# Kernel tuning notes

Hardware: AMD Instinct MI355X
Metric: run time of the kernel (lower is better)

The kernel has to match this reference:

```python
import jax, jax.numpy as jnp
import numpy as np

TAU = 1.0
K = 10
N_NODES = 1048576
N_GRAPHS = 4096


def setup_inputs() -> dict:
    key = jax.random.key(0)
    k1, k2, k3 = jax.random.split(key, 3)
    # per-node scalar logits
    x = jax.random.normal(k1, (N_NODES, 1), dtype=jnp.float32)
    # uniforms for gumbel noise, kept away from {0,1} for log stability
    uniforms = jax.random.uniform(k2, (N_NODES, 3 * K), dtype=jnp.float32,
                                  minval=1e-6, maxval=1.0 - 1e-6)
    # PyG-style ptr: B+1 cumulative offsets, ptr[0]=0, ptr[-1]=N
    cuts = jnp.sort(jax.random.randint(k3, (N_GRAPHS - 1,), 1, N_NODES))
    ptr = jnp.concatenate([jnp.zeros((1,), cuts.dtype), cuts,
                           jnp.full((1,), N_NODES, cuts.dtype)])
    return {"x": x, "uniforms": uniforms, "ptr": ptr}


def reference(x, uniforms, ptr):
    # x: [N, 1] node logits; uniforms: [N, 3k]; ptr: [B+1] segment offsets
    N = x.shape[0]
    B = ptr.shape[0] - 1
    # node i belongs to graph g where ptr[g] <= i < ptr[g+1]
    seg = jnp.searchsorted(ptr, jnp.arange(N), side="right") - 1  # [N]
    gumbel = -jnp.log(-jnp.log(uniforms))                           # [N, 3k]
    noisy = (gumbel + x) / TAU                                      # [N, 3k]
    # segmented softmax over nodes (dim=0 within each graph), per column
    m = jax.ops.segment_max(noisy, seg, num_segments=B)             # [B, 3k]
    e = jnp.exp(noisy - m[seg])                                     # [N, 3k]
    denom = jax.ops.segment_sum(e, seg, num_segments=B)             # [B, 3k]
    probs = e / denom[seg]                                          # [N, 3k]
    # max over the 3k gumbel samples per node
    samples = jnp.max(probs, axis=1)                                # [N]
    return samples[:, None]                                         # [N, 1]
```

## Files before the change

kernel.cpp:

```cpp
#include <hip/hip_runtime.h>

#define NK3 30
#define NKP 15

__device__ __forceinline__ float hw_log2(float a) { return __builtin_amdgcn_logf(a); }
__device__ __forceinline__ float hw_exp2(float a) { return __builtin_amdgcn_exp2f(a); }
__device__ __forceinline__ float hw_rcp(float a)  { return __builtin_amdgcn_rcpf(a); }

template <int CTRL>
__device__ __forceinline__ float dpp_add(float v) {
    int s = __builtin_amdgcn_update_dpp(0, __float_as_int(v), CTRL, 0xF, 0xF, true);
    return v + __int_as_float(s);
}
__device__ __forceinline__ float group16_sum(float v) {
    v = dpp_add<0xB1>(v);
    v = dpp_add<0x4E>(v);
    v = dpp_add<0x141>(v);
    v = dpp_add<0x140>(v);
    return v;
}


__global__ __launch_bounds__(256) void k1_window_sums(
    const float* __restrict__ x, const float* __restrict__ uniforms,
    float* __restrict__ wp16, int N)
{
    const int wid  = (blockIdx.x << 2) + (threadIdx.x >> 6);
    const int lane = threadIdx.x & 63;
    const int base0 = wid << 8;
    if (base0 >= N) return;

    for (int c = 0; c < 4; ++c) {
        const int base = base0 + (c << 6);
        if (base >= N) return;
        const int n  = base + lane;
        const int nv = (n < N) ? n : (N - 1);

        const float2* row = reinterpret_cast<const float2*>(uniforms + (size_t)nv * NK3);
        float2 u[NKP];
#pragma unroll
        for (int k = 0; k < NKP; ++k) u[k] = row[k];
        float E = hw_exp2(x[nv] * 1.44269504f);
        E = (n < N) ? E : 0.0f;

        float r[NK3];
#pragma unroll
        for (int k = 0; k < NKP; ++k) {
            r[2 * k]     = E * hw_rcp(-hw_log2(u[k].x));
            r[2 * k + 1] = E * hw_rcp(-hw_log2(u[k].y));
        }

#pragma unroll
        for (int j = 0; j < NK3; ++j) r[j] = group16_sum(r[j]);

        if ((lane & 15) == 0) {
            float* dst = wp16 + ((size_t)(base >> 4) + (lane >> 4)) * NK3;
#pragma unroll
            for (int j = 0; j < NK3; ++j) dst[j] = r[j];
        }
    }
}

__global__ __launch_bounds__(256) void k2_segment_den(
    const float* __restrict__ x, const float* __restrict__ uniforms,
    const int* __restrict__ ptr, const float* __restrict__ wp16,
    float* __restrict__ den, int B)
{
    const int s = (blockIdx.x << 2) + (threadIdx.x >> 6);
    if (s >= B) return;
    const int lane = threadIdx.x & 63;
    const int h  = lane >> 5;
    const int j  = lane & 31;
    const bool jact = (j < NK3);
    const int jc = jact ? j : 0;

    const int start = ptr[s];
    const int end   = ptr[s + 1];

    const int wlo = (start + 15) >> 4;
    const int whi = end >> 4;
    const int head_end = min(wlo << 4, end);
    const int tail_beg = max(whi << 4, head_end);

    float acc = 0.0f;

    for (int w = wlo + h; w < whi; w += 2)
        acc += wp16[(size_t)w * NK3 + jc];

    for (int n = start + h; n < head_end; n += 2) {
        const float E = hw_exp2(x[n] * 1.44269504f);
        const float uv = uniforms[(size_t)n * NK3 + jc];
        acc = fmaf(E, hw_rcp(-hw_log2(uv)), acc);
    }
    for (int n = tail_beg + h; n < end; n += 2) {
        const float E = hw_exp2(x[n] * 1.44269504f);
        const float uv = uniforms[(size_t)n * NK3 + jc];
        acc = fmaf(E, hw_rcp(-hw_log2(uv)), acc);
    }

    acc += __shfl_xor(acc, 32, 64);

    if (h == 0 && jact) den[(size_t)s * NK3 + j] = acc;
}

__global__ __launch_bounds__(256) void k3_output(
    const float* __restrict__ x, const float* __restrict__ uniforms,
    const int* __restrict__ ptr, const float* __restrict__ den,
    float* __restrict__ out, int N, int B)
{
    const int wid  = (blockIdx.x << 2) + (threadIdx.x >> 6);
    const int lane = threadIdx.x & 63;
    const int base = wid << 8;
    if (base >= N) return;

    const int n0 = base + lane;
    int lo = 0, hi = B;
    while (hi - lo > 1) { int mid = (lo + hi) >> 1; if (ptr[mid] <= n0) lo = mid; else hi = mid; }
    int seg = lo;

    int cur = -1;
    float l[NK3];

    for (int c = 0; c < 4; ++c) {
        const int n = base + (c << 6) + lane;
        if (n >= N) return;
        while (n >= ptr[seg + 1]) ++seg;

        if (seg != cur) {
            cur = seg;
#pragma unroll
            for (int j = 0; j < NK3; ++j) l[j] = hw_rcp(den[(size_t)seg * NK3 + j]);
        }

        const float2* row = reinterpret_cast<const float2*>(uniforms + (size_t)n * NK3);
        float mx = 0.0f;
#pragma unroll
        for (int k = 0; k < NKP; ++k) {
            const float2 u = row[k];
            const float r0 = hw_rcp(-hw_log2(u.x));
            const float r1 = hw_rcp(-hw_log2(u.y));
            mx = fmaxf(mx, fmaxf(r0 * l[2 * k], r1 * l[2 * k + 1]));
        }
        out[n] = hw_exp2(x[n] * 1.44269504f) * mx;
    }
}

__global__ __launch_bounds__(256) void gnn_fallback(
    const float* __restrict__ x, const float* __restrict__ uniforms,
    const int* __restrict__ ptr, float* __restrict__ out)
{
    const int wave = threadIdx.x >> 6;
    const int lane = threadIdx.x & 63;
    const int g = (blockIdx.x << 2) + wave;
    const int start = ptr[g];
    const int end   = ptr[g + 1];
    if (end <= start) return;

    float acc[NK3];
#pragma unroll
    for (int j = 0; j < NK3; ++j) acc[j] = 0.0f;
    const int iters = (end - start + 63) >> 6;

    for (int it = 0; it < iters; ++it) {
        const int n = start + (it << 6) + lane;
        if (n < end) {
            const float E = hw_exp2(x[n] * 1.44269504f);
            const float2* row = reinterpret_cast<const float2*>(uniforms + (size_t)n * NK3);
#pragma unroll
            for (int k = 0; k < NKP; ++k) {
                float2 u = row[k];
                acc[2 * k]     = fmaf(E, hw_rcp(-hw_log2(u.x)), acc[2 * k]);
                acc[2 * k + 1] = fmaf(E, hw_rcp(-hw_log2(u.y)), acc[2 * k + 1]);
            }
        }
    }
#pragma unroll
    for (int j = 0; j < NK3; ++j) {
        float v = acc[j];
#pragma unroll
        for (int off = 1; off < 64; off <<= 1) v += __shfl_xor(v, off, 64);
        acc[j] = hw_rcp(v);
    }
    for (int it = 0; it < iters; ++it) {
        const int n = start + (it << 6) + lane;
        if (n < end) {
            const float2* row = reinterpret_cast<const float2*>(uniforms + (size_t)n * NK3);
            float mx = 0.0f;
#pragma unroll
            for (int k = 0; k < NKP; ++k) {
                float2 u = row[k];
                const float r0 = hw_rcp(-hw_log2(u.x));
                const float r1 = hw_rcp(-hw_log2(u.y));
                mx = fmaxf(mx, fmaxf(r0 * acc[2 * k], r1 * acc[2 * k + 1]));
            }
            out[n] = hw_exp2(x[n] * 1.44269504f) * mx;
        }
    }
}

extern "C" void kernel_launch(void* const* d_in, const int* in_sizes, int n_in,
                              void* d_out, int out_size, void* d_ws, size_t ws_size,
                              hipStream_t stream) {
    const float* x        = (const float*)d_in[0];
    const float* uniforms = (const float*)d_in[1];
    const int*   ptr      = (const int*)d_in[2];
    float* out = (float*)d_out;

    const int N = in_sizes[0];
    const int B = in_sizes[2] - 1;
    const int NW16 = (N + 15) / 16;
    const size_t ws_needed = ((size_t)NW16 + (size_t)B) * NK3 * sizeof(float);

    if (ws_size >= ws_needed && d_ws != nullptr) {
        float* wp16 = (float*)d_ws;
        float* den  = wp16 + (size_t)NW16 * NK3;

        const int b1 = (N + 1023) / 1024;
        k1_window_sums<<<b1, 256, 0, stream>>>(x, uniforms, wp16, N);

        const int b2 = (B + 3) / 4;
        k2_segment_den<<<b2, 256, 0, stream>>>(x, uniforms, ptr, wp16, den, B);

        const int b3 = (N + 1023) / 1024;
        k3_output<<<b3, 256, 0, stream>>>(x, uniforms, ptr, den, out, N, B);
    } else {
        const int blocks = (B + 3) / 4;
        gnn_fallback<<<blocks, 256, 0, stream>>>(x, uniforms, ptr, out);
    }
}
```

Measured before the change: 70.23 us.

## Give each wave one 64-node chunk and precompute reciprocal denominators

k1 and k3 now have each wave handle a single 64-node chunk instead of looping over four, which launches four times as many blocks so more loads are in flight and more wavefronts are available to hide latency. k2 stores reciprocals of the segment denominators, so k3 no longer computes 30 reciprocals per segment change. In k3, every thread now does a full binary search over ptr and loads its segment's reciprocal row itself, instead of walking forward from a cached segment. This adds redundant ptr and rden reads, mostly served from cache.

```diff
diff --git a/kernel.cpp b/kernel.cpp
--- a/kernel.cpp
+++ b/kernel.cpp
@@ -25,46 +25,42 @@
     const float* __restrict__ x, const float* __restrict__ uniforms,
     float* __restrict__ wp16, int N)
 {
-    const int wid  = (blockIdx.x << 2) + (threadIdx.x >> 6);
-    const int lane = threadIdx.x & 63;
-    const int base0 = wid << 8;
-    if (base0 >= N) return;
-
-    for (int c = 0; c < 4; ++c) {
-        const int base = base0 + (c << 6);
-        if (base >= N) return;
-        const int n  = base + lane;
-        const int nv = (n < N) ? n : (N - 1);
-
-        const float2* row = reinterpret_cast<const float2*>(uniforms + (size_t)nv * NK3);
-        float2 u[NKP];
-#pragma unroll
-        for (int k = 0; k < NKP; ++k) u[k] = row[k];
-        float E = hw_exp2(x[nv] * 1.44269504f);
-        E = (n < N) ? E : 0.0f;
-
-        float r[NK3];
-#pragma unroll
-        for (int k = 0; k < NKP; ++k) {
-            r[2 * k]     = E * hw_rcp(-hw_log2(u[k].x));
-            r[2 * k + 1] = E * hw_rcp(-hw_log2(u[k].y));
-        }
-
-#pragma unroll
-        for (int j = 0; j < NK3; ++j) r[j] = group16_sum(r[j]);
-
-        if ((lane & 15) == 0) {
-            float* dst = wp16 + ((size_t)(base >> 4) + (lane >> 4)) * NK3;
-#pragma unroll
-            for (int j = 0; j < NK3; ++j) dst[j] = r[j];
-        }
+    const int w    = (blockIdx.x << 2) + (threadIdx.x >> 6);
+    const int lane = threadIdx.x & 63;
+    const int base = w << 6;
+    if (base >= N) return;
+
+    const int n  = base + lane;
+    const int nv = (n < N) ? n : (N - 1);
+
+    const float2* row = reinterpret_cast<const float2*>(uniforms + (size_t)nv * NK3);
+    float2 u[NKP];
+#pragma unroll
+    for (int k = 0; k < NKP; ++k) u[k] = row[k];
+    float E = hw_exp2(x[nv] * 1.44269504f);
+    E = (n < N) ? E : 0.0f;
+
+    float r[NK3];
+#pragma unroll
+    for (int k = 0; k < NKP; ++k) {
+        r[2 * k]     = E * hw_rcp(-hw_log2(u[k].x));
+        r[2 * k + 1] = E * hw_rcp(-hw_log2(u[k].y));
+    }
+
+#pragma unroll
+    for (int j = 0; j < NK3; ++j) r[j] = group16_sum(r[j]);
+
+    if ((lane & 15) == 0) {
+        float* dst = wp16 + ((size_t)(base >> 4) + (lane >> 4)) * NK3;
+#pragma unroll
+        for (int j = 0; j < NK3; ++j) dst[j] = r[j];
     }
 }
 
 __global__ __launch_bounds__(256) void k2_segment_den(
     const float* __restrict__ x, const float* __restrict__ uniforms,
     const int* __restrict__ ptr, const float* __restrict__ wp16,
-    float* __restrict__ den, int B)
+    float* __restrict__ rden, int B)
 {
     const int s = (blockIdx.x << 2) + (threadIdx.x >> 6);
     if (s >= B) return;
@@ -100,49 +96,40 @@
 
     acc += __shfl_xor(acc, 32, 64);
 
-    if (h == 0 && jact) den[(size_t)s * NK3 + j] = acc;
+    if (h == 0 && jact) rden[(size_t)s * NK3 + j] = hw_rcp(acc);
 }
 
 __global__ __launch_bounds__(256) void k3_output(
     const float* __restrict__ x, const float* __restrict__ uniforms,
-    const int* __restrict__ ptr, const float* __restrict__ den,
+    const int* __restrict__ ptr, const float* __restrict__ rden,
     float* __restrict__ out, int N, int B)
 {
     const int wid  = (blockIdx.x << 2) + (threadIdx.x >> 6);
     const int lane = threadIdx.x & 63;
-    const int base = wid << 8;
-    if (base >= N) return;
-
-    const int n0 = base + lane;
+    const int n = (wid << 6) + lane;
+    if (n >= N) return;
+
     int lo = 0, hi = B;
-    while (hi - lo > 1) { int mid = (lo + hi) >> 1; if (ptr[mid] <= n0) lo = mid; else hi = mid; }
-    int seg = lo;
-
-    int cur = -1;
-    float l[NK3];
-
-    for (int c = 0; c < 4; ++c) {
-        const int n = base + (c << 6) + lane;
-        if (n >= N) return;
-        while (n >= ptr[seg + 1]) ++seg;
-
-        if (seg != cur) {
-            cur = seg;
-#pragma unroll
-            for (int j = 0; j < NK3; ++j) l[j] = hw_rcp(den[(size_t)seg * NK3 + j]);
-        }
-
-        const float2* row = reinterpret_cast<const float2*>(uniforms + (size_t)n * NK3);
-        float mx = 0.0f;
-#pragma unroll
-        for (int k = 0; k < NKP; ++k) {
-            const float2 u = row[k];
-            const float r0 = hw_rcp(-hw_log2(u.x));
-            const float r1 = hw_rcp(-hw_log2(u.y));
-            mx = fmaxf(mx, fmaxf(r0 * l[2 * k], r1 * l[2 * k + 1]));
-        }
-        out[n] = hw_exp2(x[n] * 1.44269504f) * mx;
-    }
+    while (hi - lo > 1) { int mid = (lo + hi) >> 1; if (ptr[mid] <= n) lo = mid; else hi = mid; }
+    const int seg = lo;
+
+    const float2* row = reinterpret_cast<const float2*>(uniforms + (size_t)n * NK3);
+    const float2* lr  = reinterpret_cast<const float2*>(rden + (size_t)seg * NK3);
+
+    float2 u[NKP], l[NKP];
+#pragma unroll
+    for (int k = 0; k < NKP; ++k) u[k] = row[k];
+#pragma unroll
+    for (int k = 0; k < NKP; ++k) l[k] = lr[k];
+
+    float mx = 0.0f;
+#pragma unroll
+    for (int k = 0; k < NKP; ++k) {
+        const float r0 = hw_rcp(-hw_log2(u[k].x));
+        const float r1 = hw_rcp(-hw_log2(u[k].y));
+        mx = fmaxf(mx, fmaxf(r0 * l[k].x, r1 * l[k].y));
+    }
+    out[n] = hw_exp2(x[n] * 1.44269504f) * mx;
 }
 
 __global__ __launch_bounds__(256) void gnn_fallback(
@@ -213,16 +200,17 @@
 
     if (ws_size >= ws_needed && d_ws != nullptr) {
         float* wp16 = (float*)d_ws;
-        float* den  = wp16 + (size_t)NW16 * NK3;
-
-        const int b1 = (N + 1023) / 1024;
+        float* rden = wp16 + (size_t)NW16 * NK3;
+
+        const int NW64 = (N + 63) / 64;
+        const int b1 = (NW64 + 3) / 4;
         k1_window_sums<<<b1, 256, 0, stream>>>(x, uniforms, wp16, N);
 
         const int b2 = (B + 3) / 4;
-        k2_segment_den<<<b2, 256, 0, stream>>>(x, uniforms, ptr, wp16, den, B);
-
-        const int b3 = (N + 1023) / 1024;
-        k3_output<<<b3, 256, 0, stream>>>(x, uniforms, ptr, den, out, N, B);
+        k2_segment_den<<<b2, 256, 0, stream>>>(x, uniforms, ptr, wp16, rden, B);
+
+        const int b3 = (NW64 + 3) / 4;
+        k3_output<<<b3, 256, 0, stream>>>(x, uniforms, ptr, rden, out, N, B);
     } else {
         const int blocks = (B + 3) / 4;
         gnn_fallback<<<blocks, 256, 0, stream>>>(x, uniforms, ptr, out);
```

Measured after the change: 72.51 us, median of 2. +3.2%, slower.
